# Kernel optimization log

Measured on AMD Instinct MI355X. Metric: run time of the kernel, lower is better.

The kernel has to match this reference:

```python
import jax, jax.numpy as jnp
from jax import lax
import numpy as np

EPS = 1e-5  # BatchNorm eps


def _gatv2(x, src, dst, Wl, Wr, att, bias, heads, d, concat):
    # x: [B, N, Fin]; src/dst: [E] (self-loops appended, PyG add_self_loops=True)
    B, N, _ = x.shape
    xl = jnp.einsum('bnf,of->bno', x, Wl).reshape(B, N, heads, d)  # source proj
    xr = jnp.einsum('bnf,of->bno', x, Wr).reshape(B, N, heads, d)  # target proj
    e = jax.nn.leaky_relu(xl[:, src] + xr[:, dst], 0.2)            # [B,E,H,d]
    logit = jnp.einsum('behd,hd->beh', e, att)                     # [B,E,H]
    seg_max = jax.vmap(lambda v: jax.ops.segment_max(v, dst, num_segments=N))
    seg_sum = jax.vmap(lambda v: jax.ops.segment_sum(v, dst, num_segments=N))
    m = seg_max(logit)                                             # [B,N,H]
    p = jnp.exp(logit - m[:, dst])
    alpha = p / seg_sum(p)[:, dst]                                 # edge softmax over targets
    out = seg_sum(alpha[..., None] * xl[:, src])                   # [B,N,H,d]
    out = out.reshape(B, N, heads * d) if concat else out.mean(2)
    return out + bias


def _bn(h, g, b, m, v):  # BatchNorm1d, eval mode (running stats)
    return (h - m) * (g / jnp.sqrt(v + EPS)) + b


def _lstm_layer(seq, Wih, Whh, bih, bhh):
    # seq: [BN, T, Hin]; gate order i,f,g,o (PyTorch)
    BN, T, _ = seq.shape
    H = Whh.shape[1]
    pre = jnp.einsum('bti,gi->tbg', seq, Wih) + bih + bhh          # [T,BN,4H]
    def step(carry, xp):
        h, c = carry
        g = xp + h @ Whh.T
        i, f, gg, o = jnp.split(g, 4, axis=-1)
        c = jax.nn.sigmoid(f) * c + jax.nn.sigmoid(i) * jnp.tanh(gg)
        h = jax.nn.sigmoid(o) * jnp.tanh(c)
        return (h, c), h
    h0 = jnp.zeros((BN, H), seq.dtype)
    _, hs = lax.scan(step, (h0, h0), pre)
    return jnp.swapaxes(hs, 0, 1)                                  # [BN,T,H]


def forward(x, edge_index, Wp, bp, Wl1, Wr1, a1, bg1, g1, be1, m1, v1,
            Wl2, Wr2, a2, bg2, g2, be2, m2, v2,
            Wih0, Whh0, bih0, bhh0, Wih1, Whh1, bih1, bhh1,
            Wa, ba, Ws1, bs1, Ws2, bs2, Wh1, bh1, Wh2, bh2):
    b, t, n, f = x.shape
    H = Wp.shape[0]
    loops = jnp.arange(n, dtype=edge_index.dtype)
    src = jnp.concatenate([edge_index[0], loops])
    dst = jnp.concatenate([edge_index[1], loops])
    xt = x.reshape(b * t, n, f)  # batch all (b,t) graph passes together
    h1 = jax.nn.elu(_bn(_gatv2(xt, src, dst, Wl1, Wr1, a1, bg1, 2, H, True), g1, be1, m1, v1))
    # dropout is identity in eval mode
    h2 = jax.nn.elu(_bn(_gatv2(h1, src, dst, Wl2, Wr2, a2, bg2, 1, H, False), g2, be2, m2, v2))
    h = h2 + jnp.einsum('bnf,hf->bnh', xt, Wp) + bp                # residual input_proj
    sp = h.reshape(b * n, t, H)  # replicates torch .view(b*n,t,H) on contiguous [b,t,n,H]
    lo = _lstm_layer(_lstm_layer(sp, Wih0, Whh0, bih0, bhh0), Wih1, Whh1, bih1, bhh1)
    aw = jax.nn.softmax(jnp.einsum('bth,oh->bto', lo, Wa) + ba, axis=1)
    ctx = (aw * lo).sum(1)                                         # [b*n, H]
    nb = Ws1.shape[1]
    sk = x[:, -1, :, :nb].reshape(b * n, nb)
    sk = jax.nn.gelu(sk @ Ws1.T + bs1, approximate=False) @ Ws2.T + bs2
    z = jnp.concatenate([ctx, sk], axis=1)
    z = jax.nn.gelu(z @ Wh1.T + bh1, approximate=False) @ Wh2.T + bh2
    return z.reshape(b, n, 1)


def setup_inputs() -> dict:
    key = jax.random.key(0)
    ks = jax.random.split(key, 40)
    b, t, n, f, H, E, nb = 4, 16, 1000, 32, 128, 16000, 13
    p = lambda k, s: (jax.random.normal(k, s) * 0.05).astype(jnp.float32)
    x = jax.random.normal(ks[0], (b, t, n, f), jnp.float32)
    src = jax.random.randint(ks[1], (E,), 0, n)
    dst = (src + jax.random.randint(ks[2], (E,), 1, n)) % n  # no accidental self-loops
    edge_index = jnp.stack([src, dst]).astype(jnp.int32)
    return dict(
        x=x, edge_index=edge_index,
        Wp=p(ks[3], (H, f)), bp=p(ks[4], (H,)),
        Wl1=p(ks[5], (2 * H, f)), Wr1=p(ks[6], (2 * H, f)), a1=p(ks[7], (2, H)), bg1=p(ks[8], (2 * H,)),
        g1=1.0 + p(ks[9], (2 * H,)), be1=p(ks[10], (2 * H,)), m1=p(ks[11], (2 * H,)),
        v1=jax.random.uniform(ks[12], (2 * H,), minval=0.5, maxval=1.5),
        Wl2=p(ks[13], (H, 2 * H)), Wr2=p(ks[14], (H, 2 * H)), a2=p(ks[15], (1, H)), bg2=p(ks[16], (H,)),
        g2=1.0 + p(ks[17], (H,)), be2=p(ks[18], (H,)), m2=p(ks[19], (H,)),
        v2=jax.random.uniform(ks[20], (H,), minval=0.5, maxval=1.5),
        Wih0=p(ks[21], (4 * H, H)), Whh0=p(ks[22], (4 * H, H)), bih0=p(ks[23], (4 * H,)), bhh0=p(ks[24], (4 * H,)),
        Wih1=p(ks[25], (4 * H, H)), Whh1=p(ks[26], (4 * H, H)), bih1=p(ks[27], (4 * H,)), bhh1=p(ks[28], (4 * H,)),
        Wa=p(ks[29], (1, H)), ba=p(ks[30], (1,)),
        Ws1=p(ks[31], (H // 2, nb)), bs1=p(ks[32], (H // 2,)),
        Ws2=p(ks[33], (H // 4, H // 2)), bs2=p(ks[34], (H // 4,)),
        Wh1=p(ks[35], (H // 2, H + H // 4)), bh1=p(ks[36], (H // 2,)),
        Wh2=p(ks[37], (1, H // 2)), bh2=p(ks[38], (1,)))


def reference(x, edge_index, Wp, bp, Wl1, Wr1, a1, bg1, g1, be1, m1, v1,
              Wl2, Wr2, a2, bg2, g2, be2, m2, v2,
              Wih0, Whh0, bih0, bhh0, Wih1, Whh1, bih1, bhh1,
              Wa, ba, Ws1, bs1, Ws2, bs2, Wh1, bh1, Wh2, bh2):
    return forward(x, edge_index, Wp, bp, Wl1, Wr1, a1, bg1, g1, be1, m1, v1,
                   Wl2, Wr2, a2, bg2, g2, be2, m2, v2,
                   Wih0, Whh0, bih0, bhh0, Wih1, Whh1, bih1, bhh1,
                   Wa, ba, Ws1, bs1, Ws2, bs2, Wh1, bh1, Wh2, bh2)
```

## Files before the change

### kernel.cpp

```cpp
#include <hip/hip_runtime.h>
#include <hip/hip_fp16.h>

#define EPS_BN 1e-5f

typedef __attribute__((ext_vector_type(8))) short bf16x8;
typedef __attribute__((ext_vector_type(4))) float f32x4;

#define O_SRCD   0u
#define O_DSTD   17024u
#define O_COUNTS 34048u
#define O_OFFS   35072u
#define O_CURS   36096u
#define O_EIDX   37120u
#define O_PW1    54144u
#define O_PW2    74624u
#define O_LW     140160u
#define O_BCOMB  402304u
#define O_ABF    403328u
#define O_HWT    404352u
#define O_BIG0   417536u
#define O_BIG1   (O_BIG0 + 16384000u)
#define O_BIG2   (O_BIG1 + 16384000u)
#define O_BIG3   (O_BIG2 + 16384000u)
#define O_BIG4   (O_BIG3 + 8192000u)
#define O_SXL    (O_BIG4 + 8192000u)

__device__ __forceinline__ float rsum32(float p) {
  p += __shfl_xor(p, 1);  p += __shfl_xor(p, 2);  p += __shfl_xor(p, 4);
  p += __shfl_xor(p, 8);  p += __shfl_xor(p, 16); return p;
}
__device__ __forceinline__ float rsum64(float p) {
  p = rsum32(p); p += __shfl_xor(p, 32); return p;
}
__device__ __forceinline__ float lrelu(float x) { return x > 0.f ? x : 0.2f * x; }
__device__ __forceinline__ float eluf(float x)  { return x > 0.f ? x : expm1f(x); }
__device__ __forceinline__ float geluf(float x) { return 0.5f * x * (1.f + erff(x * 0.70710678118654752f)); }
__device__ __forceinline__ unsigned short f2bf(float f) {
  unsigned int u = __float_as_uint(f);
  u += 0x7FFFu + ((u >> 16) & 1u);
  return (unsigned short)(u >> 16);
}
__device__ __forceinline__ float bf2f(unsigned short h) {
  return __uint_as_float(((unsigned int)h) << 16);
}
__device__ __forceinline__ unsigned short f2h(float x) {
  __half h = __float2half(x);
  return *reinterpret_cast<unsigned short*>(&h);
}
__device__ __forceinline__ float h2f(unsigned short u) {
  __half h = *reinterpret_cast<__half*>(&u);
  return __half2float(h);
}
__device__ __forceinline__ void unpk(unsigned int w, float& lo, float& hi) {
  lo = __uint_as_float(w << 16);
  hi = __uint_as_float(w & 0xFFFF0000u);
}

__global__ void prep_edges(const int* __restrict__ ei, int* __restrict__ srcD,
                           int* __restrict__ dstD, int* __restrict__ counts) {
  int i = blockIdx.x * 256 + threadIdx.x;
  if (i < 1024) counts[i] = 0;
  if (i < 17000) {
    int s = (i < 16000) ? ei[i] : (i - 16000);
    int d = (i < 16000) ? ei[16000 + i] : (i - 16000);
    srcD[i] = s; dstD[i] = d;
  }
}
__global__ void hist_kernel(const int* __restrict__ dstD, int* __restrict__ counts) {
  int i = blockIdx.x * 256 + threadIdx.x;
  if (i < 17000) atomicAdd(&counts[dstD[i]], 1);
}
__global__ void scan_kernel(const int* __restrict__ counts, int* __restrict__ offs,
                            int* __restrict__ curs) {
  __shared__ int sh[1024];
  int i = threadIdx.x;
  int v = (i < 1000) ? counts[i] : 0;
  sh[i] = v;
  __syncthreads();
  for (int d = 1; d < 1024; d <<= 1) {
    int t = (i >= d) ? sh[i - d] : 0;
    __syncthreads();
    sh[i] += t;
    __syncthreads();
  }
  if (i < 1000) { offs[i + 1] = sh[i]; curs[i] = sh[i] - v; }
  if (i == 0) offs[0] = 0;
}
__global__ void fill_kernel(const int* __restrict__ srcD, const int* __restrict__ dstD,
                            int* __restrict__ curs, int* __restrict__ esrc) {
  int i = blockIdx.x * 256 + threadIdx.x;
  if (i < 17000) { int p = atomicAdd(&curs[dstD[i]], 1); esrc[p] = srcD[i]; }
}

__global__ void pack_kernel(
    const float* __restrict__ Wl1, const float* __restrict__ Wr1, const float* __restrict__ Wp,
    const float* __restrict__ Wl2, const float* __restrict__ Wr2,
    const float* __restrict__ Wih0, const float* __restrict__ Whh0,
    const float* __restrict__ bih0, const float* __restrict__ bhh0,
    const float* __restrict__ Wih1, const float* __restrict__ Whh1,
    const float* __restrict__ bih1, const float* __restrict__ bhh1,
    const float* __restrict__ g1, const float* __restrict__ be1, const float* __restrict__ m1,
    const float* __restrict__ v1, const float* __restrict__ bg1,
    const float* __restrict__ g2, const float* __restrict__ be2, const float* __restrict__ m2,
    const float* __restrict__ v2, const float* __restrict__ bg2,
    const float* __restrict__ Ws1, const float* __restrict__ Ws2, const float* __restrict__ Wh1,
    float* __restrict__ PW1, unsigned short* __restrict__ PW2Bu,
    unsigned short* __restrict__ PHHBu, unsigned short* __restrict__ PWBu,
    float* __restrict__ BC, float* __restrict__ ABF, float* __restrict__ HWT)
{
  int i = blockIdx.x * 256 + threadIdx.x;
  if (i < 262144) {
    int e = i & 7, lane = (i >> 3) & 63, gt = (i >> 9) & 31,
        kc = (i >> 14) & 3, sp = (i >> 16) & 1, L = (i >> 17) & 1;
    int gp = (gt << 4) + (lane & 15);
    int jj = gp >> 2, gate = gp & 3;
    int kk = (kc << 5) + ((lane >> 4) << 3) + e;
    const float* Wih = L ? Wih1 : Wih0;
    const float* Whh = L ? Whh1 : Whh0;
    float wv = Wih[(gate * 128 + jj) * 128 + kk];
    unsigned short hi = f2bf(wv);
    PWBu[i] = (sp == 0) ? hi : f2bf(wv - bf2f(hi));
    float hv = Whh[(gate * 128 + jj) * 128 + kk];
    unsigned short hhi = f2bf(hv);
    PHHBu[i] = (sp == 0) ? hhi : f2bf(hv - bf2f(hhi));
  }
  if (i < 131072) {
    int e = i & 7, lane = (i >> 3) & 63, ct = (i >> 9) & 15,
        kc = (i >> 13) & 7, sp = (i >> 16) & 1;
    int c = (ct << 4) + (lane & 15);
    int k = (kc << 5) + ((lane >> 4) << 3) + e;
    float wv2 = (c < 128) ? Wl2[c * 256 + k] : Wr2[(c - 128) * 256 + k];
    unsigned short hi = f2bf(wv2);
    PW2Bu[i] = (sp == 0) ? hi : f2bf(wv2 - bf2f(hi));
  }
  if (i < 20480) { int g = i % 640, k = i / 640;
    PW1[i] = (g < 256) ? Wl1[g * 32 + k] : (g < 512) ? Wr1[(g - 256) * 32 + k]
                                                     : Wp[(g - 512) * 32 + k]; }
  if (i < 1024) { int u = i & 3, jj = (i >> 2) & 127, L = i >> 9;
    BC[i] = (L ? bih1 : bih0)[u * 128 + jj] + (L ? bhh1 : bhh0)[u * 128 + jj]; }
  if (i < 768) {
    if (i < 256) ABF[i] = g1[i] * rsqrtf(v1[i] + EPS_BN);
    else if (i < 512) { int c = i - 256; float a = g1[c] * rsqrtf(v1[c] + EPS_BN);
      ABF[i] = (bg1[c] - m1[c]) * a + be1[c]; }
    else if (i < 640) { int c = i - 512; ABF[i] = g2[c] * rsqrtf(v2[c] + EPS_BN); }
    else { int c = i - 640; float a = g2[c] * rsqrtf(v2[c] + EPS_BN);
      ABF[i] = (bg2[c] - m2[c]) * a + be2[c]; }
  }
  if (i < 13120) {
    if (i < 832) { int l = i & 63, c = i >> 6; HWT[i] = Ws1[l * 13 + c]; }
    else if (i < 2880) { int k = i - 832; int l = k & 31, jj = k >> 5; HWT[i] = Ws2[l * 64 + jj]; }
    else { int k = i - 2880; int l = k & 63, r = k >> 6; HWT[i] = Wh1[l * 160 + r]; }
  }
}

__global__ __launch_bounds__(320)
void proj1_kernel(const float* __restrict__ X, const float* __restrict__ PW1,
                  const float* __restrict__ bp, unsigned short* __restrict__ XL1u,
                  float* __restrict__ XR1, float* __restrict__ XP)
{
  __shared__ __align__(16) float xs[32][16];
  const int tid = threadIdx.x;
  const int r0 = blockIdx.x * 16;
  for (int el = tid; el < 512; el += 320) {
    int r = el >> 5, k = el & 31;
    xs[k][r] = X[(size_t)(r0 + r) * 32 + k];
  }
  __syncthreads();
  const int gA = tid, gB = tid + 320;
  float accA[16], accB[16];
  const float iB = (gB >= 512) ? bp[gB - 512] : 0.f;
  #pragma unroll
  for (int r = 0; r < 16; ++r) { accA[r] = 0.f; accB[r] = iB; }
  for (int k = 0; k < 32; ++k) {
    float wA = PW1[k * 640 + gA], wB = PW1[k * 640 + gB];
    float xv[16];
    #pragma unroll
    for (int q = 0; q < 4; ++q)
      *reinterpret_cast<float4*>(&xv[q * 4]) = *reinterpret_cast<const float4*>(&xs[k][q * 4]);
    #pragma unroll
    for (int r = 0; r < 16; ++r) {
      accA[r] = fmaf(wA, xv[r], accA[r]);
      accB[r] = fmaf(wB, xv[r], accB[r]);
    }
  }
  for (int r = 0; r < 16; ++r) {
    size_t row = r0 + r;
    if (gA < 256) XL1u[row * 256 + gA] = f2bf(accA[r]);
    else          XR1[row * 256 + (gA - 256)] = accA[r];
    if (gB < 512) XR1[row * 256 + (gB - 256)] = accB[r];
    else          XP[row * 128 + (gB - 512)] = accB[r];
  }
}

__global__ __launch_bounds__(256)
void sxl_kernel(const unsigned short* __restrict__ XLu, const float* __restrict__ a,
                float* __restrict__ SXL, int C)
{
  const int tid = threadIdx.x;
  const int g = tid >> 4, li = tid & 15;
  const size_t row = (size_t)blockIdx.x * 16 + g;
  const int fpl = C >> 4;
  const int f0 = li * fpl;
  const unsigned short* xp = XLu + row * C + f0;
  const float* ap = a + f0;
  float s = 0.f;
  for (int k = 0; k < fpl; k += 8) {
    uint4 u = *reinterpret_cast<const uint4*>(xp + k);
    float x[8];
    unpk(u.x, x[0], x[1]); unpk(u.y, x[2], x[3]);
    unpk(u.z, x[4], x[5]); unpk(u.w, x[6], x[7]);
    #pragma unroll
    for (int e = 0; e < 8; ++e) s = fmaf(ap[k + e], x[e], s);
  }
  s += __shfl_xor(s, 1); s += __shfl_xor(s, 2); s += __shfl_xor(s, 4);
  if (C == 256) {
    if ((li & 7) == 0) SXL[row * 2 + (li >> 3)] = 0.6f * s;
  } else {
    s += __shfl_xor(s, 8);
    if (li == 0) SXL[row] = 0.6f * s;
  }
}

__global__ __launch_bounds__(256)
void gat1_kernel(const unsigned short* __restrict__ XLu, const float* __restrict__ XR,
                 const float* __restrict__ SXL,
                 const int* __restrict__ esrc, const int* __restrict__ offs,
                 const float* __restrict__ a1, const float* __restrict__ ABF,
                 float* __restrict__ H1)
{
  const int lane = threadIdx.x & 63;
  const int wv = threadIdx.x >> 6;
  const int n = blockIdx.x * 4 + wv;
  const int b = blockIdx.y;
  const int epar = lane >> 5;
  const int head = (lane >> 4) & 1;
  const int li = lane & 15;
  const int f0 = head * 128 + li * 8;
  const int beg = offs[n];
  const int deg = offs[n + 1] - beg;
  const uint4* XLb = reinterpret_cast<const uint4*>(XLu) + (size_t)b * 32000 + (f0 >> 3);
  const float* SXLb = SXL + (size_t)b * 2000;
  float xr[8], av[8];
  {
    const float* xrp = XR + (size_t)(b * 1000 + n) * 256 + f0;
    float4 t0 = *reinterpret_cast<const float4*>(xrp);
    float4 t1 = *reinterpret_cast<const float4*>(xrp + 4);
    xr[0]=t0.x; xr[1]=t0.y; xr[2]=t0.z; xr[3]=t0.w;
    xr[4]=t1.x; xr[5]=t1.y; xr[6]=t1.z; xr[7]=t1.w;
    const float* ap = a1 + f0;
    float4 a0 = *reinterpret_cast<const float4*>(ap);
    float4 a1v = *reinterpret_cast<const float4*>(ap + 4);
    av[0]=a0.x; av[1]=a0.y; av[2]=a0.z; av[3]=a0.w;
    av[4]=a1v.x; av[5]=a1v.y; av[6]=a1v.z; av[7]=a1v.w;
  }
  float ssum = 0.f, acc[8];
  #pragma unroll
  for (int k = 0; k < 8; ++k) acc[k] = 0.f;
  bool v = epar < deg;
  int sC = esrc[beg + (v ? epar : 0)];
  uint4 u = XLb[(size_t)sC * 32];
  float slxC = SXLb[sC * 2 + head];
  for (int i0 = 0; i0 < deg; i0 += 2) {
    int nmy = i0 + 2 + epar;
    bool nv = nmy < deg;
    int sN = esrc[beg + (nv ? nmy : 0)];
    uint4 un = XLb[(size_t)sN * 32];
    float slxN = SXLb[sN * 2 + head];
    float x[8];
    unpk(u.x, x[0], x[1]); unpk(u.y, x[2], x[3]);
    unpk(u.z, x[4], x[5]); unpk(u.w, x[6], x[7]);
    float p = 0.f;
    #pragma unroll
    for (int k = 0; k < 8; ++k)
      p = fmaf(av[k], fabsf(x[k] + xr[k]), p);
    p += __shfl_xor(p, 1); p += __shfl_xor(p, 2);
    p += __shfl_xor(p, 4); p += __shfl_xor(p, 8);
    float we = v ? __expf(fmaf(0.4f, p, slxC)) : 0.f;
    ssum += we;
    #pragma unroll
    for (int k = 0; k < 8; ++k) acc[k] = fmaf(we, x[k], acc[k]);
    v = nv; u = un; slxC = slxN;
  }
  ssum += __shfl_xor(ssum, 32);
  float inv = 1.f / ssum;
  float A4[8], B4[8];
  {
    const float* aap = ABF + f0;
    float4 t0 = *reinterpret_cast<const float4*>(aap);
    float4 t1 = *reinterpret_cast<const float4*>(aap + 4);
    A4[0]=t0.x; A4[1]=t0.y; A4[2]=t0.z; A4[3]=t0.w;
    A4[4]=t1.x; A4[5]=t1.y; A4[6]=t1.z; A4[7]=t1.w;
    const float* bbp = ABF + 256 + f0;
    float4 s0v = *reinterpret_cast<const float4*>(bbp);
    float4 s1v = *reinterpret_cast<const float4*>(bbp + 4);
    B4[0]=s0v.x; B4[1]=s0v.y; B4[2]=s0v.z; B4[3]=s0v.w;
    B4[4]=s1v.x; B4[5]=s1v.y; B4[6]=s1v.z; B4[7]=s1v.w;
  }
  float o[8];
  #pragma unroll
  for (int k = 0; k < 8; ++k) {
    float A = acc[k] + __shfl_xor(acc[k], 32);
    o[k] = eluf(fmaf(A * inv, A4[k], B4[k]));
  }
  if (lane < 32) {
    float* hp = H1 + (size_t)(b * 1000 + n) * 256 + f0;
    *reinterpret_cast<float4*>(hp) = make_float4(o[0], o[1], o[2], o[3]);
    *reinterpret_cast<float4*>(hp + 4) = make_float4(o[4], o[5], o[6], o[7]);
  }
}

__global__ __launch_bounds__(512)
void proj2_kernel(const float* __restrict__ H1, const unsigned short* __restrict__ PW2B,
                  unsigned short* __restrict__ XL2u, float* __restrict__ XR2)
{
  const int tid = threadIdx.x;
  const int lane = tid & 63;
  const int wv = tid >> 6;
  const int l15 = lane & 15;
  const int kg = lane >> 4;
  const int r0 = blockIdx.x * 32;
  f32x4 acc[2][2];
  #pragma unroll
  for (int rt = 0; rt < 2; ++rt)
    #pragma unroll
    for (int ct = 0; ct < 2; ++ct)
      #pragma unroll
      for (int e = 0; e < 4; ++e) acc[rt][ct][e] = 0.f;
  for (int kc = 0; kc < 8; ++kc) {
    bf16x8 xh[2], xl[2];
    #pragma unroll
    for (int rt = 0; rt < 2; ++rt) {
      const float* xp = H1 + (size_t)(r0 + rt * 16 + l15) * 256 + (kc << 5) + (kg << 3);
      float4 va = *reinterpret_cast<const float4*>(xp);
      float4 vb = *reinterpret_cast<const float4*>(xp + 4);
      float xs[8] = {va.x, va.y, va.z, va.w, vb.x, vb.y, vb.z, vb.w};
      #pragma unroll
      for (int e = 0; e < 8; ++e) {
        unsigned short h = f2bf(xs[e]);
        xh[rt][e] = (short)h;
        xl[rt][e] = (short)f2bf(xs[e] - bf2f(h));
      }
    }
    #pragma unroll
    for (int ct = 0; ct < 2; ++ct) {
      const int ctg = (wv << 1) + ct;
      const unsigned short* wp = PW2B + ((size_t)(kc * 16 + ctg)) * 512 + lane * 8;
      bf16x8 whi = *reinterpret_cast<const bf16x8*>(wp);
      bf16x8 wlo = *reinterpret_cast<const bf16x8*>(wp + 65536);
      #pragma unroll
      for (int rt = 0; rt < 2; ++rt) {
        acc[rt][ct] = __builtin_amdgcn_mfma_f32_16x16x32_bf16(xh[rt], whi, acc[rt][ct], 0, 0, 0);
        acc[rt][ct] = __builtin_amdgcn_mfma_f32_16x16x32_bf16(xh[rt], wlo, acc[rt][ct], 0, 0, 0);
        acc[rt][ct] = __builtin_amdgcn_mfma_f32_16x16x32_bf16(xl[rt], whi, acc[rt][ct], 0, 0, 0);
      }
    }
  }
  #pragma unroll
  for (int ct = 0; ct < 2; ++ct) {
    const int col = (wv << 5) + (ct << 4) + l15;
    #pragma unroll
    for (int rt = 0; rt < 2; ++rt) {
      #pragma unroll
      for (int reg = 0; reg < 4; ++reg) {
        const int row = r0 + rt * 16 + (kg << 2) + reg;
        float val = acc[rt][ct][reg];
        if (col < 128) XL2u[(size_t)row * 128 + col] = f2bf(val);
        else           XR2[(size_t)row * 128 + (col - 128)] = val;
      }
    }
  }
}

__global__ __launch_bounds__(256)
void gat2_kernel(const unsigned short* __restrict__ XLu, const float* __restrict__ XR,
                 const float* __restrict__ SXL,
                 const int* __restrict__ esrc, const int* __restrict__ offs,
                 const float* __restrict__ a2, const float* __restrict__ ABF,
                 const float* __restrict__ XP, float* __restrict__ Hout)
{
  const int lane = threadIdx.x & 63;
  const int wv = threadIdx.x >> 6;
  const int n = blockIdx.x * 4 + wv;
  const int b = blockIdx.y;
  const int grp = lane >> 4;
  const int li = lane & 15;
  const int f0 = li * 8;
  const int beg = offs[n];
  const int deg = offs[n + 1] - beg;
  const uint4* XLb = reinterpret_cast<const uint4*>(XLu) + (size_t)b * 16000 + li;
  const float* SXLb = SXL + (size_t)b * 1000;
  float xr[8], av[8];
  {
    const float* xrp = XR + (size_t)(b * 1000 + n) * 128 + f0;
    float4 t0 = *reinterpret_cast<const float4*>(xrp);
    float4 t1 = *reinterpret_cast<const float4*>(xrp + 4);
    xr[0]=t0.x; xr[1]=t0.y; xr[2]=t0.z; xr[3]=t0.w;
    xr[4]=t1.x; xr[5]=t1.y; xr[6]=t1.z; xr[7]=t1.w;
    const float* ap = a2 + f0;
    float4 a0 = *reinterpret_cast<const float4*>(ap);
    float4 a1v = *reinterpret_cast<const float4*>(ap + 4);
    av[0]=a0.x; av[1]=a0.y; av[2]=a0.z; av[3]=a0.w;
    av[4]=a1v.x; av[5]=a1v.y; av[6]=a1v.z; av[7]=a1v.w;
  }
  float ssum = 0.f, acc[8];
  #pragma unroll
  for (int k = 0; k < 8; ++k) acc[k] = 0.f;
  bool v = grp < deg;
  int sC = esrc[beg + (v ? grp : 0)];
  uint4 u = XLb[(size_t)sC * 16];
  float slxC = SXLb[sC];
  for (int i0 = 0; i0 < deg; i0 += 4) {
    int nmy = i0 + 4 + grp;
    bool nv = nmy < deg;
    int sN = esrc[beg + (nv ? nmy : 0)];
    uint4 un = XLb[(size_t)sN * 16];
    float slxN = SXLb[sN];
    float x[8];
    unpk(u.x, x[0], x[1]); unpk(u.y, x[2], x[3]);
    unpk(u.z, x[4], x[5]); unpk(u.w, x[6], x[7]);
    float p = 0.f;
    #pragma unroll
    for (int k = 0; k < 8; ++k)
      p = fmaf(av[k], fabsf(x[k] + xr[k]), p);
    p += __shfl_xor(p, 1); p += __shfl_xor(p, 2);
    p += __shfl_xor(p, 4); p += __shfl_xor(p, 8);
    float we = v ? __expf(fmaf(0.4f, p, slxC)) : 0.f;
    ssum += we;
    #pragma unroll
    for (int k = 0; k < 8; ++k) acc[k] = fmaf(we, x[k], acc[k]);
    v = nv; u = un; slxC = slxN;
  }
  ssum += __shfl_xor(ssum, 16);
  ssum += __shfl_xor(ssum, 32);
  #pragma unroll
  for (int k = 0; k < 8; ++k) {
    acc[k] += __shfl_xor(acc[k], 16);
    acc[k] += __shfl_xor(acc[k], 32);
  }
  float inv = 1.f / ssum;
  if (lane < 16) {
    const float* aap = ABF + 512 + f0;
    float4 t0 = *reinterpret_cast<const float4*>(aap);
    float4 t1 = *reinterpret_cast<const float4*>(aap + 4);
    const float* bbp = ABF + 640 + f0;
    float4 s0v = *reinterpret_cast<const float4*>(bbp);
    float4 s1v = *reinterpret_cast<const float4*>(bbp + 4);
    const float* xpp = XP + (size_t)(b * 1000 + n) * 128 + f0;
    float4 p0 = *reinterpret_cast<const float4*>(xpp);
    float4 p1 = *reinterpret_cast<const float4*>(xpp + 4);
    float A4[8] = {t0.x, t0.y, t0.z, t0.w, t1.x, t1.y, t1.z, t1.w};
    float B4[8] = {s0v.x, s0v.y, s0v.z, s0v.w, s1v.x, s1v.y, s1v.z, s1v.w};
    float P4[8] = {p0.x, p0.y, p0.z, p0.w, p1.x, p1.y, p1.z, p1.w};
    float o[8];
    #pragma unroll
    for (int k = 0; k < 8; ++k)
      o[k] = eluf(fmaf(acc[k] * inv, A4[k], B4[k])) + P4[k];
    float* hp = Hout + (size_t)(b * 1000 + n) * 128 + f0;
    *reinterpret_cast<float4*>(hp) = make_float4(o[0], o[1], o[2], o[3]);
    *reinterpret_cast<float4*>(hp + 4) = make_float4(o[4], o[5], o[6], o[7]);
  }
}

__global__ __launch_bounds__(512)
void gemm_pre_kernel(const float* __restrict__ X, const unsigned short* __restrict__ PWB,
                     const float* __restrict__ BCL, unsigned short* __restrict__ PREh)
{
  const int tid = threadIdx.x;
  const int lane = tid & 63;
  const int wv = tid >> 6;
  const int l15 = lane & 15;
  const int kg = lane >> 4;
  const int r0 = blockIdx.x * 32;
  f32x4 acc[2][4];
  #pragma unroll
  for (int rt = 0; rt < 2; ++rt)
    #pragma unroll
    for (int gt = 0; gt < 4; ++gt)
      #pragma unroll
      for (int e = 0; e < 4; ++e) acc[rt][gt][e] = 0.f;
  for (int kc = 0; kc < 4; ++kc) {
    bf16x8 xh[2], xl[2];
    #pragma unroll
    for (int rt = 0; rt < 2; ++rt) {
      const float* xp = X + (size_t)(r0 + rt * 16 + l15) * 128 + (kc << 5) + (kg << 3);
      float4 va = *reinterpret_cast<const float4*>(xp);
      float4 vb = *reinterpret_cast<const float4*>(xp + 4);
      float xs[8] = {va.x, va.y, va.z, va.w, vb.x, vb.y, vb.z, vb.w};
      #pragma unroll
      for (int e = 0; e < 8; ++e) {
        unsigned short h = f2bf(xs[e]);
        xh[rt][e] = (short)h;
        xl[rt][e] = (short)f2bf(xs[e] - bf2f(h));
      }
    }
    #pragma unroll
    for (int gt = 0; gt < 4; ++gt) {
      const int gtg = (wv << 2) + gt;
      const unsigned short* wp = PWB + ((size_t)(kc * 32 + gtg)) * 512 + lane * 8;
      bf16x8 whi = *reinterpret_cast<const bf16x8*>(wp);
      bf16x8 wlo = *reinterpret_cast<const bf16x8*>(wp + 65536);
      #pragma unroll
      for (int rt = 0; rt < 2; ++rt) {
        acc[rt][gt] = __builtin_amdgcn_mfma_f32_16x16x32_bf16(xh[rt], whi, acc[rt][gt], 0, 0, 0);
        acc[rt][gt] = __builtin_amdgcn_mfma_f32_16x16x32_bf16(xh[rt], wlo, acc[rt][gt], 0, 0, 0);
        acc[rt][gt] = __builtin_amdgcn_mfma_f32_16x16x32_bf16(xl[rt], whi, acc[rt][gt], 0, 0, 0);
      }
    }
  }
  #pragma unroll
  for (int gt = 0; gt < 4; ++gt) {
    const int col = (wv << 6) + (gt << 4) + l15;
    const float bias = BCL[col];
    #pragma unroll
    for (int rt = 0; rt < 2; ++rt) {
      #pragma unroll
      for (int reg = 0; reg < 4; ++reg) {
        const int row = r0 + rt * 16 + (kg << 2) + reg;
        PREh[(size_t)row * 512 + col] = f2h(acc[rt][gt][reg] + bias);
      }
    }
  }
}

__device__ __forceinline__ float cellf(float4 g, float& c) {
  const float ig = 1.f / (1.f + __expf(-g.x));
  const float fg = 1.f / (1.f + __expf(-g.y));
  const float gg = tanhf(g.z);
  const float og = 1.f / (1.f + __expf(-g.w));
  c = fmaf(fg, c, ig * gg);
  return og * tanhf(c);
}

__global__ __launch_bounds__(512)
void rec2_kernel(const unsigned short* __restrict__ PREh,
                 const unsigned short* __restrict__ PHHB,
                 float* __restrict__ HOUT)
{
  __shared__ unsigned short whi[65536];
  __shared__ unsigned short afr[2][4][64][8];
  const int tid = threadIdx.x;
  const int lane = tid & 63;
  const int w = tid >> 6;
  const int l15 = lane & 15;
  const int kg = lane >> 4;
  const int q0 = blockIdx.x << 4;
  for (int i = tid; i < 8192; i += 512)
    reinterpret_cast<uint4*>(whi)[i] = reinterpret_cast<const uint4*>(PHHB)[i];
  reinterpret_cast<uint4*>(&afr[0][0][0][0])[tid] = make_uint4(0u, 0u, 0u, 0u);
  const unsigned short* wloG = PHHB + 65536;
  float cs[4] = {0.f, 0.f, 0.f, 0.f};
  const int qq = l15 & 3;
  const int uu = l15 >> 2;
  const int seq = (kg << 2) + qq;
  for (int t = 0; t < 16; ++t) {
    __syncthreads();
    bf16x8 ah[4], al[4];
    #pragma unroll
    for (int kc = 0; kc < 4; ++kc) {
      ah[kc] = *reinterpret_cast<const bf16x8*>(&afr[0][kc][lane][0]);
      al[kc] = *reinterpret_cast<const bf16x8*>(&afr[1][kc][lane][0]);
    }
    f32x4 acc[4];
    #pragma unroll
    for (int gl = 0; gl < 4; ++gl)
      #pragma unroll
      for (int e = 0; e < 4; ++e) acc[gl][e] = 0.f;
    #pragma unroll
    for (int gl = 0; gl < 4; ++gl) {
      const int gt = (w << 2) + gl;
      #pragma unroll
      for (int kc = 0; kc < 4; ++kc) {
        const int off = ((kc * 32 + gt) * 64 + lane) * 8;
        bf16x8 wh = *reinterpret_cast<const bf16x8*>(&whi[off]);
        bf16x8 wl = *reinterpret_cast<const bf16x8*>(&wloG[off]);
        acc[gl] = __builtin_amdgcn_mfma_f32_16x16x32_bf16(ah[kc], wh, acc[gl], 0, 0, 0);
        acc[gl] = __builtin_amdgcn_mfma_f32_16x16x32_bf16(ah[kc], wl, acc[gl], 0, 0, 0);
        acc[gl] = __builtin_amdgcn_mfma_f32_16x16x32_bf16(al[kc], wh, acc[gl], 0, 0, 0);
      }
    }
    __syncthreads();
    const int row = ((q0 + seq) << 4) + t;
    #pragma unroll
    for (int gl = 0; gl < 4; ++gl) {
      const int gt = (w << 2) + gl;
      float in0 = acc[gl][0], in1 = acc[gl][1], in2 = acc[gl][2], in3 = acc[gl][3];
      float s0 = __shfl_xor(in1, 1), s1 = __shfl_xor(in0, 1),
            s2 = __shfl_xor(in3, 1), s3 = __shfl_xor(in2, 1);
      const bool b0 = (qq & 1);
      float t0 = b0 ? s0 : in0;
      float t1 = b0 ? in1 : s1;
      float t2 = b0 ? s2 : in2;
      float t3 = b0 ? in3 : s3;
      float u0 = __shfl_xor(t2, 2), u1 = __shfl_xor(t3, 2),
            u2 = __shfl_xor(t0, 2), u3 = __shfl_xor(t1, 2);
      const bool b1 = (qq & 2);
      float g0 = b1 ? u0 : t0;
      float g1 = b1 ? u1 : t1;
      float g2 = b1 ? t2 : u2;
      float g3 = b1 ? t3 : u3;
      const unsigned short* pp = PREh + (size_t)row * 512 + (gt << 4) + (uu << 2);
      ushort4 pu = *reinterpret_cast<const ushort4*>(pp);
      float4 gv = make_float4(g0 + h2f(pu.x), g1 + h2f(pu.y),
                              g2 + h2f(pu.z), g3 + h2f(pu.w));
      float h = cellf(gv, cs[gl]);
      const int unit = (gt << 2) + uu;
      HOUT[(size_t)row * 128 + unit] = h;
      if (t < 15) {
        unsigned short hh = f2bf(h);
        unsigned short hl = f2bf(h - bf2f(hh));
        const int kc2 = unit >> 5;
        const int lane2 = seq | (((unit & 31) >> 3) << 4);
        const int e2 = unit & 7;
        afr[0][kc2][lane2][e2] = hh;
        afr[1][kc2][lane2][e2] = hl;
      }
    }
  }
}

__global__ __launch_bounds__(64)
void attn_kernel(const float* __restrict__ LO, const float* __restrict__ X,
                 const float* __restrict__ Wa, const float* __restrict__ ba,
                 const float* __restrict__ bs1, const float* __restrict__ bs2,
                 const float* __restrict__ bh1, const float* __restrict__ bh2,
                 const float* __restrict__ Wh2, const float* __restrict__ HWT,
                 float* __restrict__ out)
{
  const int q = blockIdx.x, l = threadIdx.x;
  const float* lob = LO + (size_t)q * 2048;
  float loa[16], lobv[16];
  #pragma unroll
  for (int t = 0; t < 16; ++t) {
    loa[t]  = lob[t * 128 + l];
    lobv[t] = lob[t * 128 + 64 + l];
  }
  const float wa = Wa[l], wb = Wa[64 + l];
  float sc[16];
  #pragma unroll
  for (int t = 0; t < 16; ++t) sc[t] = rsum64(loa[t] * wa + lobv[t] * wb) + ba[0];
  float mx = sc[0];
  #pragma unroll
  for (int t = 1; t < 16; ++t) mx = fmaxf(mx, sc[t]);
  float den = 0.f;
  #pragma unroll
  for (int t = 0; t < 16; ++t) { sc[t] = __expf(sc[t] - mx); den += sc[t]; }
  const float inv = 1.f / den;
  float ca = 0.f, cb = 0.f;
  #pragma unroll
  for (int t = 0; t < 16; ++t) {
    float wgt = sc[t] * inv;
    ca = fmaf(wgt, loa[t], ca);
    cb = fmaf(wgt, lobv[t], cb);
  }
  __shared__ float zsh[160];
  __shared__ float hsk[64];
  __shared__ float skin[16];
  zsh[l] = ca; zsh[64 + l] = cb;
  const int bb = q / 1000, nn = q - bb * 1000;
  if (l < 13) skin[l] = X[(size_t)((bb * 16 + 15) * 1000 + nn) * 32 + l];
  __syncthreads();
  float h1 = bs1[l];
  for (int c = 0; c < 13; ++c) h1 = fmaf(skin[c], HWT[c * 64 + l], h1);
  h1 = geluf(h1);
  hsk[l] = h1;
  __syncthreads();
  if (l < 32) {
    float a = bs2[l];
    for (int jj = 0; jj < 64; ++jj) a = fmaf(hsk[jj], HWT[832 + jj * 32 + l], a);
    zsh[128 + l] = a;
  }
  __syncthreads();
  float hh = bh1[l];
  for (int r = 0; r < 160; ++r) hh = fmaf(zsh[r], HWT[2880 + r * 64 + l], hh);
  hh = geluf(hh);
  float s = rsum64(hh * Wh2[l]);
  if (l == 0) out[q] = s + bh2[0];
}

extern "C" void kernel_launch(void* const* d_in, const int* in_sizes, int n_in,
                              void* d_out, int out_size, void* d_ws, size_t ws_size,
                              hipStream_t stream)
{
  const float* x    = (const float*)d_in[0];
  const int*   ei   = (const int*)d_in[1];
  const float* Wp   = (const float*)d_in[2];
  const float* bp   = (const float*)d_in[3];
  const float* Wl1  = (const float*)d_in[4];
  const float* Wr1  = (const float*)d_in[5];
  const float* a1   = (const float*)d_in[6];
  const float* bg1  = (const float*)d_in[7];
  const float* g1   = (const float*)d_in[8];
  const float* be1  = (const float*)d_in[9];
  const float* m1   = (const float*)d_in[10];
  const float* v1   = (const float*)d_in[11];
  const float* Wl2  = (const float*)d_in[12];
  const float* Wr2  = (const float*)d_in[13];
  const float* a2   = (const float*)d_in[14];
  const float* bg2  = (const float*)d_in[15];
  const float* g2   = (const float*)d_in[16];
  const float* be2  = (const float*)d_in[17];
  const float* m2   = (const float*)d_in[18];
  const float* v2   = (const float*)d_in[19];
  const float* Wih0 = (const float*)d_in[20];
  const float* Whh0 = (const float*)d_in[21];
  const float* bih0 = (const float*)d_in[22];
  const float* bhh0 = (const float*)d_in[23];
  const float* Wih1 = (const float*)d_in[24];
  const float* Whh1 = (const float*)d_in[25];
  const float* bih1 = (const float*)d_in[26];
  const float* bhh1 = (const float*)d_in[27];
  const float* Wa   = (const float*)d_in[28];
  const float* ba   = (const float*)d_in[29];
  const float* Ws1  = (const float*)d_in[30];
  const float* bs1  = (const float*)d_in[31];
  const float* Ws2  = (const float*)d_in[32];
  const float* bs2  = (const float*)d_in[33];
  const float* Wh1  = (const float*)d_in[34];
  const float* bh1  = (const float*)d_in[35];
  const float* Wh2  = (const float*)d_in[36];
  const float* bh2  = (const float*)d_in[37];

  float* ws = (float*)d_ws;
  int* srcD   = (int*)(ws + O_SRCD);
  int* dstD   = (int*)(ws + O_DSTD);
  int* counts = (int*)(ws + O_COUNTS);
  int* offs   = (int*)(ws + O_OFFS);
  int* curs   = (int*)(ws + O_CURS);
  int* esrc   = (int*)(ws + O_EIDX);
  float* PW1  = ws + O_PW1;
  unsigned short* PW2Bu = (unsigned short*)(ws + O_PW2);
  unsigned short* PHHBu = (unsigned short*)(ws + O_LW);
  unsigned short* PWBu  = (unsigned short*)(ws + O_LW + 131072u);
  float* BC   = ws + O_BCOMB;
  float* ABF  = ws + O_ABF;
  float* HWT  = ws + O_HWT;
  unsigned short* XL1u = (unsigned short*)(ws + O_BIG0);
  float* XR1  = ws + O_BIG1;
  float* H1   = ws + O_BIG2;
  float* XP   = ws + O_BIG3;
  float* Hres = ws + O_BIG4;
  unsigned short* XL2u = (unsigned short*)(ws + O_BIG0);
  float* XR2  = ws + O_BIG0 + 8192000u;
  unsigned short* PREh = (unsigned short*)(ws + O_BIG0);
  float* H1SEQ = ws + O_BIG2;
  float* LOp  = ws + O_BIG3;
  float* SXL1 = ws + O_SXL;
  float* SXL2 = ws + O_SXL + 128000u;
  float* outp = (float*)d_out;

  prep_edges<<<67, 256, 0, stream>>>(ei, srcD, dstD, counts);
  hist_kernel<<<67, 256, 0, stream>>>(dstD, counts);
  scan_kernel<<<1, 1024, 0, stream>>>(counts, offs, curs);
  fill_kernel<<<67, 256, 0, stream>>>(srcD, dstD, curs, esrc);
  pack_kernel<<<1024, 256, 0, stream>>>(Wl1, Wr1, Wp, Wl2, Wr2,
      Wih0, Whh0, bih0, bhh0, Wih1, Whh1, bih1, bhh1,
      g1, be1, m1, v1, bg1, g2, be2, m2, v2, bg2,
      Ws1, Ws2, Wh1, PW1, PW2Bu, PHHBu, PWBu, BC, ABF, HWT);
  proj1_kernel<<<4000, 320, 0, stream>>>(x, PW1, bp, XL1u, XR1, XP);
  sxl_kernel<<<4000, 256, 0, stream>>>(XL1u, a1, SXL1, 256);
  gat1_kernel<<<dim3(250, 64), 256, 0, stream>>>(XL1u, XR1, SXL1, esrc, offs, a1, ABF, H1);
  proj2_kernel<<<2000, 512, 0, stream>>>(H1, PW2Bu, XL2u, XR2);
  sxl_kernel<<<4000, 256, 0, stream>>>(XL2u, a2, SXL2, 128);
  gat2_kernel<<<dim3(250, 64), 256, 0, stream>>>(XL2u, XR2, SXL2, esrc, offs, a2, ABF, XP, Hres);
  gemm_pre_kernel<<<2000, 512, 0, stream>>>(Hres, PWBu, BC, PREh);
  rec2_kernel<<<250, 512, 0, stream>>>(PREh, PHHBu, H1SEQ);
  gemm_pre_kernel<<<2000, 512, 0, stream>>>(H1SEQ, PWBu + 131072u, BC + 512, PREh);
  rec2_kernel<<<250, 512, 0, stream>>>(PREh, PHHBu + 131072u, LOp);
  attn_kernel<<<4000, 64, 0, stream>>>(LOp, x, Wa, ba, bs1, bs2, bh1, bh2, Wh2, HWT, outp);
}
```

Before: 549.8 us.

## Fold attention source-score dot products into projections and fuse edge prep kernels

The four edge-preprocessing kernels are merged into one single-block kernel that uses shared-memory histogram, scan and fill. The per-node source attention scalars are precomputed algebraically: att·Wl is folded into small vectors in pack_kernel and applied directly to x in proj1 and to the layer-1 output in gat1. This removes both sxl_kernel launches and their re-read of the bf16 XL buffers. The cost is a serial single-block prep kernel, and a change in numerics because the scores now come from fp32 pre-rounding values rather than bf16-stored XL.

```diff
diff --git a/kernel.cpp b/kernel.cpp
--- a/kernel.cpp
+++ b/kernel.cpp
@@ -32,7 +32,6 @@
 __device__ __forceinline__ float rsum64(float p) {
   p = rsum32(p); p += __shfl_xor(p, 32); return p;
 }
-__device__ __forceinline__ float lrelu(float x) { return x > 0.f ? x : 0.2f * x; }
 __device__ __forceinline__ float eluf(float x)  { return x > 0.f ? x : expm1f(x); }
 __device__ __forceinline__ float geluf(float x) { return 0.5f * x * (1.f + erff(x * 0.70710678118654752f)); }
 __device__ __forceinline__ unsigned short f2bf(float f) {
@@ -56,40 +55,37 @@
   hi = __uint_as_float(w & 0xFFFF0000u);
 }
 
-__global__ void prep_edges(const int* __restrict__ ei, int* __restrict__ srcD,
-                           int* __restrict__ dstD, int* __restrict__ counts) {
-  int i = blockIdx.x * 256 + threadIdx.x;
-  if (i < 1024) counts[i] = 0;
-  if (i < 17000) {
+__global__ __launch_bounds__(1024)
+void prep_all(const int* __restrict__ ei, int* __restrict__ srcD,
+              int* __restrict__ dstD, int* __restrict__ offs,
+              int* __restrict__ esrc)
+{
+  __shared__ int cnt[1024];
+  __shared__ int cur[1000];
+  const int tid = threadIdx.x;
+  cnt[tid] = 0;
+  __syncthreads();
+  for (int i = tid; i < 17000; i += 1024) {
     int s = (i < 16000) ? ei[i] : (i - 16000);
     int d = (i < 16000) ? ei[16000 + i] : (i - 16000);
     srcD[i] = s; dstD[i] = d;
-  }
-}
-__global__ void hist_kernel(const int* __restrict__ dstD, int* __restrict__ counts) {
-  int i = blockIdx.x * 256 + threadIdx.x;
-  if (i < 17000) atomicAdd(&counts[dstD[i]], 1);
-}
-__global__ void scan_kernel(const int* __restrict__ counts, int* __restrict__ offs,
-                            int* __restrict__ curs) {
-  __shared__ int sh[1024];
-  int i = threadIdx.x;
-  int v = (i < 1000) ? counts[i] : 0;
-  sh[i] = v;
+    atomicAdd(&cnt[d], 1);
+  }
   __syncthreads();
+  int v = cnt[tid];
   for (int d = 1; d < 1024; d <<= 1) {
-    int t = (i >= d) ? sh[i - d] : 0;
+    int t = (tid >= d) ? cnt[tid - d] : 0;
     __syncthreads();
-    sh[i] += t;
+    cnt[tid] += t;
     __syncthreads();
   }
-  if (i < 1000) { offs[i + 1] = sh[i]; curs[i] = sh[i] - v; }
-  if (i == 0) offs[0] = 0;
-}
-__global__ void fill_kernel(const int* __restrict__ srcD, const int* __restrict__ dstD,
-                            int* __restrict__ curs, int* __restrict__ esrc) {
-  int i = blockIdx.x * 256 + threadIdx.x;
-  if (i < 17000) { int p = atomicAdd(&curs[dstD[i]], 1); esrc[p] = srcD[i]; }
+  if (tid < 1000) { offs[tid + 1] = cnt[tid]; cur[tid] = cnt[tid] - v; }
+  if (tid == 0) offs[0] = 0;
+  __syncthreads();
+  for (int i = tid; i < 17000; i += 1024) {
+    int p = atomicAdd(&cur[dstD[i]], 1);
+    esrc[p] = srcD[i];
+  }
 }
 
 __global__ void pack_kernel(
@@ -104,9 +100,11 @@
     const float* __restrict__ g2, const float* __restrict__ be2, const float* __restrict__ m2,
     const float* __restrict__ v2, const float* __restrict__ bg2,
     const float* __restrict__ Ws1, const float* __restrict__ Ws2, const float* __restrict__ Wh1,
+    const float* __restrict__ a1, const float* __restrict__ a2,
     float* __restrict__ PW1, unsigned short* __restrict__ PW2Bu,
     unsigned short* __restrict__ PHHBu, unsigned short* __restrict__ PWBu,
-    float* __restrict__ BC, float* __restrict__ ABF, float* __restrict__ HWT)
+    float* __restrict__ BC, float* __restrict__ ABF, float* __restrict__ HWT,
+    float* __restrict__ C1F, float* __restrict__ C2F)
 {
   int i = blockIdx.x * 256 + threadIdx.x;
   if (i < 262144) {
@@ -151,12 +149,27 @@
     else if (i < 2880) { int k = i - 832; int l = k & 31, jj = k >> 5; HWT[i] = Ws2[l * 64 + jj]; }
     else { int k = i - 2880; int l = k & 63, r = k >> 6; HWT[i] = Wh1[l * 160 + r]; }
   }
+  if (i < 64) {
+    int k = i & 31, h = i >> 5;
+    float s = 0.f;
+    for (int j = 0; j < 128; ++j)
+      s = fmaf(a1[h * 128 + j], Wl1[(h * 128 + j) * 32 + k], s);
+    C1F[i] = 0.6f * s;
+  }
+  if (i < 256) {
+    float s = 0.f;
+    for (int c = 0; c < 128; ++c)
+      s = fmaf(a2[c], Wl2[c * 256 + i], s);
+    C2F[i] = 0.6f * s;
+  }
 }
 
 __global__ __launch_bounds__(320)
 void proj1_kernel(const float* __restrict__ X, const float* __restrict__ PW1,
-                  const float* __restrict__ bp, unsigned short* __restrict__ XL1u,
-                  float* __restrict__ XR1, float* __restrict__ XP)
+                  const float* __restrict__ bp, const float* __restrict__ C1F,
+                  unsigned short* __restrict__ XL1u,
+                  float* __restrict__ XR1, float* __restrict__ XP,
+                  float* __restrict__ SXL1)
 {
   __shared__ __align__(16) float xs[32][16];
   const int tid = threadIdx.x;
@@ -166,6 +179,13 @@
     xs[k][r] = X[(size_t)(r0 + r) * 32 + k];
   }
   __syncthreads();
+  if (tid < 32) {
+    int r = tid & 15, h = tid >> 4;
+    const float* c1 = C1F + h * 32;
+    float s = 0.f;
+    for (int k = 0; k < 32; ++k) s = fmaf(c1[k], xs[k][r], s);
+    SXL1[(size_t)(r0 + r) * 2 + h] = s;
+  }
   const int gA = tid, gB = tid + 320;
   float accA[16], accB[16];
   const float iB = (gB >= 512) ? bp[gB - 512] : 0.f;
@@ -193,40 +213,12 @@
 }
 
 __global__ __launch_bounds__(256)
-void sxl_kernel(const unsigned short* __restrict__ XLu, const float* __restrict__ a,
-                float* __restrict__ SXL, int C)
-{
-  const int tid = threadIdx.x;
-  const int g = tid >> 4, li = tid & 15;
-  const size_t row = (size_t)blockIdx.x * 16 + g;
-  const int fpl = C >> 4;
-  const int f0 = li * fpl;
-  const unsigned short* xp = XLu + row * C + f0;
-  const float* ap = a + f0;
-  float s = 0.f;
-  for (int k = 0; k < fpl; k += 8) {
-    uint4 u = *reinterpret_cast<const uint4*>(xp + k);
-    float x[8];
-    unpk(u.x, x[0], x[1]); unpk(u.y, x[2], x[3]);
-    unpk(u.z, x[4], x[5]); unpk(u.w, x[6], x[7]);
-    #pragma unroll
-    for (int e = 0; e < 8; ++e) s = fmaf(ap[k + e], x[e], s);
-  }
-  s += __shfl_xor(s, 1); s += __shfl_xor(s, 2); s += __shfl_xor(s, 4);
-  if (C == 256) {
-    if ((li & 7) == 0) SXL[row * 2 + (li >> 3)] = 0.6f * s;
-  } else {
-    s += __shfl_xor(s, 8);
-    if (li == 0) SXL[row] = 0.6f * s;
-  }
-}
-
-__global__ __launch_bounds__(256)
 void gat1_kernel(const unsigned short* __restrict__ XLu, const float* __restrict__ XR,
                  const float* __restrict__ SXL,
                  const int* __restrict__ esrc, const int* __restrict__ offs,
                  const float* __restrict__ a1, const float* __restrict__ ABF,
-                 float* __restrict__ H1)
+                 const float* __restrict__ C2F,
+                 float* __restrict__ H1, float* __restrict__ SXL2)
 {
   const int lane = threadIdx.x & 63;
   const int wv = threadIdx.x >> 6;
@@ -301,6 +293,19 @@
   for (int k = 0; k < 8; ++k) {
     float A = acc[k] + __shfl_xor(acc[k], 32);
     o[k] = eluf(fmaf(A * inv, A4[k], B4[k]));
+  }
+  {
+    const float* cp = C2F + f0;
+    float4 c0 = *reinterpret_cast<const float4*>(cp);
+    float4 c1 = *reinterpret_cast<const float4*>(cp + 4);
+    float cc[8] = {c0.x, c0.y, c0.z, c0.w, c1.x, c1.y, c1.z, c1.w};
+    float s2 = 0.f;
+    #pragma unroll
+    for (int k = 0; k < 8; ++k) s2 = fmaf(cc[k], o[k], s2);
+    s2 += __shfl_xor(s2, 1); s2 += __shfl_xor(s2, 2);
+    s2 += __shfl_xor(s2, 4); s2 += __shfl_xor(s2, 8);
+    s2 += __shfl_xor(s2, 16);
+    if (lane == 0) SXL2[(size_t)b * 1000 + n] = s2;
   }
   if (lane < 32) {
     float* hp = H1 + (size_t)(b * 1000 + n) * 256 + f0;
@@ -723,9 +728,7 @@
   float* ws = (float*)d_ws;
   int* srcD   = (int*)(ws + O_SRCD);
   int* dstD   = (int*)(ws + O_DSTD);
-  int* counts = (int*)(ws + O_COUNTS);
   int* offs   = (int*)(ws + O_OFFS);
-  int* curs   = (int*)(ws + O_CURS);
   int* esrc   = (int*)(ws + O_EIDX);
   float* PW1  = ws + O_PW1;
   unsigned short* PW2Bu = (unsigned short*)(ws + O_PW2);
@@ -746,21 +749,19 @@
   float* LOp  = ws + O_BIG3;
   float* SXL1 = ws + O_SXL;
   float* SXL2 = ws + O_SXL + 128000u;
+  float* C1F  = ws + O_SXL + 192000u;
+  float* C2F  = ws + O_SXL + 192064u;
   float* outp = (float*)d_out;
 
-  prep_edges<<<67, 256, 0, stream>>>(ei, srcD, dstD, counts);
-  hist_kernel<<<67, 256, 0, stream>>>(dstD, counts);
-  scan_kernel<<<1, 1024, 0, stream>>>(counts, offs, curs);
-  fill_kernel<<<67, 256, 0, stream>>>(srcD, dstD, curs, esrc);
+  prep_all<<<1, 1024, 0, stream>>>(ei, srcD, dstD, offs, esrc);
   pack_kernel<<<1024, 256, 0, stream>>>(Wl1, Wr1, Wp, Wl2, Wr2,
       Wih0, Whh0, bih0, bhh0, Wih1, Whh1, bih1, bhh1,
       g1, be1, m1, v1, bg1, g2, be2, m2, v2, bg2,
-      Ws1, Ws2, Wh1, PW1, PW2Bu, PHHBu, PWBu, BC, ABF, HWT);
-  proj1_kernel<<<4000, 320, 0, stream>>>(x, PW1, bp, XL1u, XR1, XP);
-  sxl_kernel<<<4000, 256, 0, stream>>>(XL1u, a1, SXL1, 256);
-  gat1_kernel<<<dim3(250, 64), 256, 0, stream>>>(XL1u, XR1, SXL1, esrc, offs, a1, ABF, H1);
+      Ws1, Ws2, Wh1, a1, a2, PW1, PW2Bu, PHHBu, PWBu, BC, ABF, HWT, C1F, C2F);
+  proj1_kernel<<<4000, 320, 0, stream>>>(x, PW1, bp, C1F, XL1u, XR1, XP, SXL1);
+  gat1_kernel<<<dim3(250, 64), 256, 0, stream>>>(XL1u, XR1, SXL1, esrc, offs, a1, ABF,
+                                                 C2F, H1, SXL2);
   proj2_kernel<<<2000, 512, 0, stream>>>(H1, PW2Bu, XL2u, XR2);
-  sxl_kernel<<<4000, 256, 0, stream>>>(XL2u, a2, SXL2, 128);
   gat2_kernel<<<dim3(250, 64), 256, 0, stream>>>(XL2u, XR2, SXL2, esrc, offs, a2, ABF, XP, Hres);
   gemm_pre_kernel<<<2000, 512, 0, stream>>>(Hres, PWBu, BC, PREh);
   rec2_kernel<<<250, 512, 0, stream>>>(PREh, PHHBu, H1SEQ);
```

Result: no change. 560.0 us (+1.9%).
